# Kernel optimization log

Hardware: AMD Instinct MI355X
Metric: run time of the kernel (lower is better)

The kernel has to match this reference:

```python
import jax, jax.numpy as jnp
import numpy as np

B = 4194304
N_CLASSES = 9
ALPHA = 1.0


def setup_inputs() -> dict:
    key = jax.random.key(0)
    k1, k2, k3, k4 = jax.random.split(key, 4)
    pred_probs = jax.random.normal(k1, (B, N_CLASSES), dtype=jnp.float32)
    true_class = jax.random.randint(k2, (B,), 0, N_CLASSES, dtype=jnp.int64)
    pred_points = jax.random.normal(k3, (B, 1), dtype=jnp.float32)
    true_points = jax.random.normal(k4, (B, 1), dtype=jnp.float32)
    return {"pred_probs": pred_probs, "true_class": true_class,
            "pred_points": pred_points, "true_points": true_points}


def reference(pred_probs, true_class, pred_points, true_points):
    # MSE over points (mean reduction, as nn.MSELoss default)
    mse = jnp.mean((pred_points - true_points) ** 2)

    # Per-sample cross entropy: -log_softmax(pred)[true]
    logp = jax.nn.log_softmax(pred_probs, axis=-1)          # [B, C]
    ce_i = -jnp.take_along_axis(logp, true_class[:, None], axis=-1)[:, 0]  # [B]

    # dist_type == 'Absolute': weight = |argmax - true| + 1
    pred_cls = jnp.argmax(pred_probs, axis=1)
    weight = (jnp.abs(pred_cls - true_class) + 1).astype(ce_i.dtype)

    ce = jnp.sum(weight * ce_i) / pred_probs.shape[0]
    loss = mse + ALPHA * ce
    return (loss.astype(jnp.float32), mse, ce)
```

## Files before the change

kernel.cpp:

```cpp
#include <hip/hip_runtime.h>

constexpr int BN     = 4194304;
constexpr int C      = 9;
constexpr int TPB    = 256;
constexpr int TILE   = 1024;
constexpr int NTILES = BN / TILE;
constexpr int NBLK   = 1024;

__global__ __launch_bounds__(TPB) void loss_main(
    const float* __restrict__ pred_probs,
    const int*   __restrict__ true_class,
    const float* __restrict__ pred_points,
    const float* __restrict__ true_points,
    double*      __restrict__ partials)
{
    __shared__ float lds[TILE * C];
    float4* lds4 = reinterpret_cast<float4*>(lds);
    const float4* pp4 = reinterpret_cast<const float4*>(pred_probs);
    const float4* a4  = reinterpret_cast<const float4*>(pred_points);
    const float4* b4  = reinterpret_cast<const float4*>(true_points);

    const int t = threadIdx.x;
    float mse_acc = 0.f;
    float ce_acc  = 0.f;

    for (int tile = blockIdx.x; tile < NTILES; tile += gridDim.x) {
        const float4* src = pp4 + (size_t)tile * (TILE * C / 4);
        #pragma unroll
        for (int k = 0; k < 9; ++k) {
            lds4[t + k * TPB] = src[t + k * TPB];
        }
        {
            float4 a = a4[(size_t)tile * (TILE / 4) + t];
            float4 b = b4[(size_t)tile * (TILE / 4) + t];
            float d0 = a.x - b.x, d1 = a.y - b.y, d2 = a.z - b.z, d3 = a.w - b.w;
            mse_acc += d0 * d0 + d1 * d1 + d2 * d2 + d3 * d3;
        }
        __syncthreads();
        #pragma unroll
        for (int r = 0; r < TILE / TPB; ++r) {
            const int lrow = t + r * TPB;
            const int grow = tile * TILE + lrow;
            const float* row = lds + lrow * C;
            float m = row[0];
            int am = 0;
            #pragma unroll
            for (int j = 1; j < C; ++j) {
                float v = row[j];
                if (v > m) { m = v; am = j; }
            }
            float se = 0.f;
            #pragma unroll
            for (int j = 0; j < C; ++j) se += __expf(row[j] - m);
            const int tc = true_class[grow];
            const float ce_i = m + __logf(se) - row[tc];
            int d = am - tc; if (d < 0) d = -d;
            ce_acc += (float)(d + 1) * ce_i;
        }
        __syncthreads();
    }

    double mse_d = (double)mse_acc;
    double ce_d  = (double)ce_acc;
    #pragma unroll
    for (int off = 32; off > 0; off >>= 1) {
        mse_d += __shfl_down(mse_d, off, 64);
        ce_d  += __shfl_down(ce_d, off, 64);
    }
    __shared__ double wsum[(TPB / 64) * 2];
    const int wid = t >> 6;
    if ((t & 63) == 0) { wsum[wid * 2] = mse_d; wsum[wid * 2 + 1] = ce_d; }
    __syncthreads();
    if (t == 0) {
        double ms = 0.0, cs = 0.0;
        #pragma unroll
        for (int w = 0; w < TPB / 64; ++w) { ms += wsum[w * 2]; cs += wsum[w * 2 + 1]; }
        partials[(size_t)blockIdx.x * 2]     = ms;
        partials[(size_t)blockIdx.x * 2 + 1] = cs;
    }
}

__global__ __launch_bounds__(256) void loss_finalize(
    const double* __restrict__ partials, float* __restrict__ out)
{
    const int t = threadIdx.x;
    double ms = 0.0, cs = 0.0;
    for (int b = t; b < NBLK; b += 256) {
        ms += partials[(size_t)b * 2];
        cs += partials[(size_t)b * 2 + 1];
    }
    #pragma unroll
    for (int off = 32; off > 0; off >>= 1) {
        ms += __shfl_down(ms, off, 64);
        cs += __shfl_down(cs, off, 64);
    }
    __shared__ double w[8];
    const int wid = t >> 6;
    if ((t & 63) == 0) { w[wid * 2] = ms; w[wid * 2 + 1] = cs; }
    __syncthreads();
    if (t == 0) {
        double M = 0.0, Cs = 0.0;
        #pragma unroll
        for (int i = 0; i < 4; ++i) { M += w[i * 2]; Cs += w[i * 2 + 1]; }
        const double mse = M / (double)BN;
        const double ce  = Cs / (double)BN;
        out[0] = (float)(mse + ce);
        out[1] = (float)mse;
        out[2] = (float)ce;
    }
}

extern "C" void kernel_launch(void* const* d_in, const int* in_sizes, int n_in,
                              void* d_out, int out_size, void* d_ws, size_t ws_size,
                              hipStream_t stream) {
    const float* pred_probs  = (const float*)d_in[0];
    const int*   true_class  = (const int*)d_in[1];
    const float* pred_points = (const float*)d_in[2];
    const float* true_points = (const float*)d_in[3];
    float*  out      = (float*)d_out;
    double* partials = (double*)d_ws;

    loss_main<<<NBLK, TPB, 0, stream>>>(pred_probs, true_class,
                                        pred_points, true_points, partials);
    loss_finalize<<<1, 256, 0, stream>>>(partials, out);
}
```

Baseline: 37.98 us.

## Register-prefetch next tile's inputs while computing current tile from LDS

After: 72.96 us. 1.92x slower.

```diff
diff --git a/kernel.cpp b/kernel.cpp
--- a/kernel.cpp
+++ b/kernel.cpp
@@ -6,6 +6,7 @@
 constexpr int TILE   = 1024;
 constexpr int NTILES = BN / TILE;
 constexpr int NBLK   = 1024;
+constexpr int NITER  = NTILES / NBLK;
 
 __global__ __launch_bounds__(TPB) void loss_main(
     const float* __restrict__ pred_probs,
@@ -24,23 +25,54 @@
     float mse_acc = 0.f;
     float ce_acc  = 0.f;
 
-    for (int tile = blockIdx.x; tile < NTILES; tile += gridDim.x) {
+    float4 r[9];
+    float4 pa, pb;
+    int    tcn[TILE / TPB];
+
+    int tile = (int)blockIdx.x;
+    {
         const float4* src = pp4 + (size_t)tile * (TILE * C / 4);
         #pragma unroll
-        for (int k = 0; k < 9; ++k) {
-            lds4[t + k * TPB] = src[t + k * TPB];
-        }
+        for (int k = 0; k < 9; ++k) r[k] = src[t + k * TPB];
+        pa = a4[(size_t)tile * (TILE / 4) + t];
+        pb = b4[(size_t)tile * (TILE / 4) + t];
+        #pragma unroll
+        for (int rr = 0; rr < TILE / TPB; ++rr)
+            tcn[rr] = true_class[tile * TILE + t + rr * TPB];
+    }
+
+    #pragma unroll
+    for (int it = 0; it < NITER; ++it) {
+        const int next = tile + NBLK;
+
+        #pragma unroll
+        for (int k = 0; k < 9; ++k) lds4[t + k * TPB] = r[k];
+
         {
-            float4 a = a4[(size_t)tile * (TILE / 4) + t];
-            float4 b = b4[(size_t)tile * (TILE / 4) + t];
-            float d0 = a.x - b.x, d1 = a.y - b.y, d2 = a.z - b.z, d3 = a.w - b.w;
+            float d0 = pa.x - pb.x, d1 = pa.y - pb.y;
+            float d2 = pa.z - pb.z, d3 = pa.w - pb.w;
             mse_acc += d0 * d0 + d1 * d1 + d2 * d2 + d3 * d3;
         }
+        int tc_cur[TILE / TPB];
+        #pragma unroll
+        for (int rr = 0; rr < TILE / TPB; ++rr) tc_cur[rr] = tcn[rr];
+
         __syncthreads();
+
+        if (it + 1 < NITER) {
+            const float4* src = pp4 + (size_t)next * (TILE * C / 4);
+            #pragma unroll
+            for (int k = 0; k < 9; ++k) r[k] = src[t + k * TPB];
+            pa = a4[(size_t)next * (TILE / 4) + t];
+            pb = b4[(size_t)next * (TILE / 4) + t];
+            #pragma unroll
+            for (int rr = 0; rr < TILE / TPB; ++rr)
+                tcn[rr] = true_class[next * TILE + t + rr * TPB];
+        }
+
         #pragma unroll
-        for (int r = 0; r < TILE / TPB; ++r) {
-            const int lrow = t + r * TPB;
-            const int grow = tile * TILE + lrow;
+        for (int rr = 0; rr < TILE / TPB; ++rr) {
+            const int lrow = t + rr * TPB;
             const float* row = lds + lrow * C;
             float m = row[0];
             int am = 0;
@@ -52,12 +84,14 @@
             float se = 0.f;
             #pragma unroll
             for (int j = 0; j < C; ++j) se += __expf(row[j] - m);
-            const int tc = true_class[grow];
+            const int tc = tc_cur[rr];
             const float ce_i = m + __logf(se) - row[tc];
             int d = am - tc; if (d < 0) d = -d;
             ce_acc += (float)(d + 1) * ce_i;
         }
+
         __syncthreads();
+        tile = next;
     }
 
     double mse_d = (double)mse_acc;
```

## Fuse finalize into main kernel via last-block ticket and halve tile size

Applied to the files above, without the earlier changes.

Result: slower. 100.3 us (+164.2%).

```diff
diff --git a/kernel.cpp b/kernel.cpp
--- a/kernel.cpp
+++ b/kernel.cpp
@@ -3,16 +3,19 @@
 constexpr int BN     = 4194304;
 constexpr int C      = 9;
 constexpr int TPB    = 256;
-constexpr int TILE   = 1024;
+constexpr int TILE   = 512;
 constexpr int NTILES = BN / TILE;
-constexpr int NBLK   = 1024;
+constexpr int NBLK   = 2048;
+constexpr int NITER  = NTILES / NBLK;
 
 __global__ __launch_bounds__(TPB) void loss_main(
     const float* __restrict__ pred_probs,
     const int*   __restrict__ true_class,
     const float* __restrict__ pred_points,
     const float* __restrict__ true_points,
-    double*      __restrict__ partials)
+    double*      __restrict__ partials,
+    unsigned*    __restrict__ counter,
+    float*       __restrict__ out)
 {
     __shared__ float lds[TILE * C];
     float4* lds4 = reinterpret_cast<float4*>(lds);
@@ -24,24 +27,31 @@
     float mse_acc = 0.f;
     float ce_acc  = 0.f;
 
-    for (int tile = blockIdx.x; tile < NTILES; tile += gridDim.x) {
+    int tile = (int)blockIdx.x;
+    #pragma unroll
+    for (int it = 0; it < NITER; ++it, tile += NBLK) {
         const float4* src = pp4 + (size_t)tile * (TILE * C / 4);
         #pragma unroll
-        for (int k = 0; k < 9; ++k) {
-            lds4[t + k * TPB] = src[t + k * TPB];
-        }
-        {
+        for (int k = 0; k < 4; ++k) lds4[t + k * TPB] = src[t + k * TPB];
+        if (t < (TILE * C / 4) - 4 * TPB)
+            lds4[t + 4 * TPB] = src[t + 4 * TPB];
+
+        if (t < TILE / 4) {
             float4 a = a4[(size_t)tile * (TILE / 4) + t];
             float4 b = b4[(size_t)tile * (TILE / 4) + t];
-            float d0 = a.x - b.x, d1 = a.y - b.y, d2 = a.z - b.z, d3 = a.w - b.w;
+            float d0 = a.x - b.x, d1 = a.y - b.y;
+            float d2 = a.z - b.z, d3 = a.w - b.w;
             mse_acc += d0 * d0 + d1 * d1 + d2 * d2 + d3 * d3;
         }
+        const int tc0 = true_class[tile * TILE + t];
+        const int tc1 = true_class[tile * TILE + t + TPB];
+
         __syncthreads();
+
         #pragma unroll
-        for (int r = 0; r < TILE / TPB; ++r) {
-            const int lrow = t + r * TPB;
-            const int grow = tile * TILE + lrow;
-            const float* row = lds + lrow * C;
+        for (int rr = 0; rr < 2; ++rr) {
+            const float* row = lds + (t + rr * TPB) * C;
+            const int tc = rr ? tc1 : tc0;
             float m = row[0];
             int am = 0;
             #pragma unroll
@@ -52,11 +62,11 @@
             float se = 0.f;
             #pragma unroll
             for (int j = 0; j < C; ++j) se += __expf(row[j] - m);
-            const int tc = true_class[grow];
             const float ce_i = m + __logf(se) - row[tc];
             int d = am - tc; if (d < 0) d = -d;
             ce_acc += (float)(d + 1) * ce_i;
         }
+
         __syncthreads();
     }
 
@@ -68,6 +78,7 @@
         ce_d  += __shfl_down(ce_d, off, 64);
     }
     __shared__ double wsum[(TPB / 64) * 2];
+    __shared__ unsigned s_ticket;
     const int wid = t >> 6;
     if ((t & 63) == 0) { wsum[wid * 2] = mse_d; wsum[wid * 2 + 1] = ce_d; }
     __syncthreads();
@@ -77,36 +88,35 @@
         for (int w = 0; w < TPB / 64; ++w) { ms += wsum[w * 2]; cs += wsum[w * 2 + 1]; }
         partials[(size_t)blockIdx.x * 2]     = ms;
         partials[(size_t)blockIdx.x * 2 + 1] = cs;
+        __threadfence();
+        s_ticket = atomicAdd(counter, 1u);
     }
-}
+    __syncthreads();
 
-__global__ __launch_bounds__(256) void loss_finalize(
-    const double* __restrict__ partials, float* __restrict__ out)
-{
-    const int t = threadIdx.x;
-    double ms = 0.0, cs = 0.0;
-    for (int b = t; b < NBLK; b += 256) {
-        ms += partials[(size_t)b * 2];
-        cs += partials[(size_t)b * 2 + 1];
-    }
-    #pragma unroll
-    for (int off = 32; off > 0; off >>= 1) {
-        ms += __shfl_down(ms, off, 64);
-        cs += __shfl_down(cs, off, 64);
-    }
-    __shared__ double w[8];
-    const int wid = t >> 6;
-    if ((t & 63) == 0) { w[wid * 2] = ms; w[wid * 2 + 1] = cs; }
-    __syncthreads();
-    if (t == 0) {
-        double M = 0.0, Cs = 0.0;
+    if (s_ticket == NBLK - 1) {
+        __threadfence();
+        double ms = 0.0, cs = 0.0;
+        for (int b = t; b < NBLK; b += TPB) {
+            ms += partials[(size_t)b * 2];
+            cs += partials[(size_t)b * 2 + 1];
+        }
         #pragma unroll
-        for (int i = 0; i < 4; ++i) { M += w[i * 2]; Cs += w[i * 2 + 1]; }
-        const double mse = M / (double)BN;
-        const double ce  = Cs / (double)BN;
-        out[0] = (float)(mse + ce);
-        out[1] = (float)mse;
-        out[2] = (float)ce;
+        for (int off = 32; off > 0; off >>= 1) {
+            ms += __shfl_down(ms, off, 64);
+            cs += __shfl_down(cs, off, 64);
+        }
+        if ((t & 63) == 0) { wsum[wid * 2] = ms; wsum[wid * 2 + 1] = cs; }
+        __syncthreads();
+        if (t == 0) {
+            double M = 0.0, Cs = 0.0;
+            #pragma unroll
+            for (int w = 0; w < TPB / 64; ++w) { M += wsum[w * 2]; Cs += wsum[w * 2 + 1]; }
+            const double mse = M / (double)BN;
+            const double ce  = Cs / (double)BN;
+            out[0] = (float)(mse + ce);
+            out[1] = (float)mse;
+            out[2] = (float)ce;
+        }
     }
 }
 
@@ -117,10 +127,12 @@
     const int*   true_class  = (const int*)d_in[1];
     const float* pred_points = (const float*)d_in[2];
     const float* true_points = (const float*)d_in[3];
-    float*  out      = (float*)d_out;
-    double* partials = (double*)d_ws;
+    float*    out      = (float*)d_out;
+    double*   partials = (double*)d_ws;
+    unsigned* counter  = (unsigned*)((char*)d_ws + NBLK * 2 * sizeof(double));
 
+    hipMemsetAsync(counter, 0, sizeof(unsigned), stream);
     loss_main<<<NBLK, TPB, 0, stream>>>(pred_probs, true_class,
-                                        pred_points, true_points, partials);
-    loss_finalize<<<1, 256, 0, stream>>>(partials, out);
+                                        pred_points, true_points,
+                                        partials, counter, out);
 }
```

## Load four rows per thread directly into registers, dropping the LDS staging

Applied to the files above, without the earlier changes.

Result: no change. 38.52 us (+1.4%).

```diff
diff --git a/kernel.cpp b/kernel.cpp
--- a/kernel.cpp
+++ b/kernel.cpp
@@ -1,11 +1,11 @@
 #include <hip/hip_runtime.h>
 
-constexpr int BN     = 4194304;
-constexpr int C      = 9;
-constexpr int TPB    = 256;
-constexpr int TILE   = 1024;
-constexpr int NTILES = BN / TILE;
-constexpr int NBLK   = 1024;
+constexpr int BN    = 4194304;
+constexpr int C     = 9;
+constexpr int TPB   = 256;
+constexpr int RPT   = 4;
+constexpr int NBLK  = 2048;
+constexpr int NITER = BN / (RPT * TPB * NBLK);
 
 __global__ __launch_bounds__(TPB) void loss_main(
     const float* __restrict__ pred_probs,
@@ -14,9 +14,8 @@
     const float* __restrict__ true_points,
     double*      __restrict__ partials)
 {
-    __shared__ float lds[TILE * C];
-    float4* lds4 = reinterpret_cast<float4*>(lds);
     const float4* pp4 = reinterpret_cast<const float4*>(pred_probs);
+    const int4*   tc4 = reinterpret_cast<const int4*>(true_class);
     const float4* a4  = reinterpret_cast<const float4*>(pred_points);
     const float4* b4  = reinterpret_cast<const float4*>(true_points);
 
@@ -24,40 +23,53 @@
     float mse_acc = 0.f;
     float ce_acc  = 0.f;
 
-    for (int tile = blockIdx.x; tile < NTILES; tile += gridDim.x) {
-        const float4* src = pp4 + (size_t)tile * (TILE * C / 4);
+    #pragma unroll
+    for (int it = 0; it < NITER; ++it) {
+        const int g = (it * NBLK + (int)blockIdx.x) * TPB + t;
+
+        float4 v[9];
+        #pragma unroll
+        for (int k = 0; k < 9; ++k) v[k] = pp4[(size_t)g * 9 + k];
+        const int4   tc = tc4[g];
+        const float4 pa = a4[g];
+        const float4 pb = b4[g];
+
+        {
+            float d0 = pa.x - pb.x, d1 = pa.y - pb.y;
+            float d2 = pa.z - pb.z, d3 = pa.w - pb.w;
+            mse_acc += d0 * d0 + d1 * d1 + d2 * d2 + d3 * d3;
+        }
+
+        float a[36];
         #pragma unroll
         for (int k = 0; k < 9; ++k) {
-            lds4[t + k * TPB] = src[t + k * TPB];
+            a[4 * k]     = v[k].x;
+            a[4 * k + 1] = v[k].y;
+            a[4 * k + 2] = v[k].z;
+            a[4 * k + 3] = v[k].w;
         }
-        {
-            float4 a = a4[(size_t)tile * (TILE / 4) + t];
-            float4 b = b4[(size_t)tile * (TILE / 4) + t];
-            float d0 = a.x - b.x, d1 = a.y - b.y, d2 = a.z - b.z, d3 = a.w - b.w;
-            mse_acc += d0 * d0 + d1 * d1 + d2 * d2 + d3 * d3;
-        }
-        __syncthreads();
+
         #pragma unroll
-        for (int r = 0; r < TILE / TPB; ++r) {
-            const int lrow = t + r * TPB;
-            const int grow = tile * TILE + lrow;
-            const float* row = lds + lrow * C;
-            float m = row[0];
+        for (int r = 0; r < RPT; ++r) {
+            const int base = r * C;
+            const int tcr = (r == 0) ? tc.x : (r == 1) ? tc.y : (r == 2) ? tc.z : tc.w;
+            float m = a[base];
             int am = 0;
             #pragma unroll
             for (int j = 1; j < C; ++j) {
-                float v = row[j];
-                if (v > m) { m = v; am = j; }
+                float x = a[base + j];
+                if (x > m) { m = x; am = j; }
             }
             float se = 0.f;
             #pragma unroll
-            for (int j = 0; j < C; ++j) se += __expf(row[j] - m);
-            const int tc = true_class[grow];
-            const float ce_i = m + __logf(se) - row[tc];
-            int d = am - tc; if (d < 0) d = -d;
+            for (int j = 0; j < C; ++j) se += __expf(a[base + j] - m);
+            float atc = a[base];
+            #pragma unroll
+            for (int j = 1; j < C; ++j) atc = (tcr == j) ? a[base + j] : atc;
+            const float ce_i = m + __logf(se) - atc;
+            int d = am - tcr; if (d < 0) d = -d;
             ce_acc += (float)(d + 1) * ce_i;
         }
-        __syncthreads();
     }
 
     double mse_d = (double)mse_acc;
```
